# Optimization experiments

Hardware: AMD Instinct MI355X
Metric: run time of the kernel (lower is better)

The kernel has to match this reference:

```python
import jax, jax.numpy as jnp
import numpy as np

B, P, H, NO, NA = 8, 16, 32, 32, 8
D, L, NH, F = 768, 12, 12, 3072
DH = D // NH
N = P + H * (NO + NA)  # 1296
NEG = -1e9


def _rule_mask():
    # group ids: 0=task(prefix), 1=obs, 2=action; prefix timestep = -1
    g = np.concatenate([np.zeros(P, np.int32),
                        np.tile(np.concatenate([np.full(NO, 1, np.int32), np.full(NA, 2, np.int32)]), H)])
    t = np.concatenate([np.full(P, -1, np.int32), np.repeat(np.arange(H, dtype=np.int32), NO + NA)])
    ti, tj = t[:, None], t[None, :]
    # attention_rules: everyone attends ALL to task; obs/action attend CAUSAL to obs;
    # action attends CAUSAL to action; task attends ALL to task; all else NEVER.
    rules = {(0, 0): 'all', (1, 0): 'all', (2, 0): 'all',
             (1, 1): 'causal', (2, 1): 'causal', (2, 2): 'causal'}
    m = np.zeros((N, N), bool)
    for (gi, gj), r in rules.items():
        sel = (g[:, None] == gi) & (g[None, :] == gj)
        cond = np.ones((N, N), bool) if r == 'all' else (tj <= ti)
        m |= sel & cond
    return m

RULE_MASK = jnp.asarray(_rule_mask())
SCALE = np.float32(1.0 / np.sqrt(DH))


def _ln(x, s, b):
    mu = x.mean(-1, keepdims=True)
    var = ((x - mu) ** 2).mean(-1, keepdims=True)
    return (x - mu) * jax.lax.rsqrt(var + 1e-6) * s + b


def _forward(prefix_tokens, obs_tokens, act_tokens, ln1_s, ln1_b, ln2_s, ln2_b,
             wq, wk, wv, wo, bq, bk, bv, bo, w1, b1, w2, b2, lnf_s, lnf_b,
             prefix_mask, obs_mask, act_mask):
    # assemble_input_tokens: concat timestep groups on token dim, fold horizon, prepend prefix
    ts = jnp.concatenate([obs_tokens, act_tokens], axis=2).reshape(B, H * (NO + NA), D)
    x = jnp.concatenate([prefix_tokens, ts], axis=1)  # (B, N, D)
    pad = jnp.concatenate(
        [prefix_mask, jnp.concatenate([obs_mask, act_mask], axis=2).reshape(B, -1)], axis=1)
    mask = RULE_MASK[None, None] & pad[:, None, None, :]  # (B,1,N,N), broadcast over heads
    for i in range(L):
        h = _ln(x, ln1_s[i], ln1_b[i])
        q = (h @ wq[i] + bq[i]).reshape(B, N, NH, DH)
        k = (h @ wk[i] + bk[i]).reshape(B, N, NH, DH)
        v = (h @ wv[i] + bv[i]).reshape(B, N, NH, DH)
        s = jnp.einsum('bqhd,bkhd->bhqk', q, k) * SCALE
        a = jax.nn.softmax(jnp.where(mask, s, NEG), axis=-1)
        o = jnp.einsum('bhqk,bkhd->bqhd', a, v).reshape(B, N, D)
        x = x + o @ wo[i] + bo[i]
        h2 = _ln(x, ln2_s[i], ln2_b[i])
        x = x + jax.nn.gelu(h2 @ w1[i] + b1[i]) @ w2[i] + b2[i]
    return _ln(x, lnf_s, lnf_b)


def setup_inputs() -> dict:
    key = jax.random.key(0)
    ks = jax.random.split(key, 9)
    sc = 0.02
    return dict(
        prefix_tokens=jax.random.normal(ks[0], (B, P, D), jnp.float32),
        obs_tokens=jax.random.normal(ks[1], (B, H, NO, D), jnp.float32),
        act_tokens=jax.random.normal(ks[2], (B, H, NA, D), jnp.float32),
        ln1_s=jnp.ones((L, D), jnp.float32), ln1_b=jnp.zeros((L, D), jnp.float32),
        ln2_s=jnp.ones((L, D), jnp.float32), ln2_b=jnp.zeros((L, D), jnp.float32),
        wq=jax.random.normal(ks[3], (L, D, D), jnp.float32) * sc,
        wk=jax.random.normal(ks[4], (L, D, D), jnp.float32) * sc,
        wv=jax.random.normal(ks[5], (L, D, D), jnp.float32) * sc,
        wo=jax.random.normal(ks[6], (L, D, D), jnp.float32) * sc,
        bq=jnp.zeros((L, D), jnp.float32), bk=jnp.zeros((L, D), jnp.float32),
        bv=jnp.zeros((L, D), jnp.float32), bo=jnp.zeros((L, D), jnp.float32),
        w1=jax.random.normal(ks[7], (L, D, F), jnp.float32) * sc,
        b1=jnp.zeros((L, F), jnp.float32),
        w2=jax.random.normal(ks[8], (L, F, D), jnp.float32) * sc,
        b2=jnp.zeros((L, D), jnp.float32),
        lnf_s=jnp.ones((D,), jnp.float32), lnf_b=jnp.zeros((D,), jnp.float32),
        prefix_mask=jnp.ones((B, P), bool),
        obs_mask=jnp.ones((B, H, NO), bool),
        act_mask=jnp.ones((B, H, NA), bool),
    )


def reference(prefix_tokens, obs_tokens, act_tokens, ln1_s, ln1_b, ln2_s, ln2_b,
              wq, wk, wv, wo, bq, bk, bv, bo, w1, b1, w2, b2, lnf_s, lnf_b,
              prefix_mask, obs_mask, act_mask):
    return _forward(prefix_tokens, obs_tokens, act_tokens, ln1_s, ln1_b, ln2_s, ln2_b,
                    wq, wk, wv, wo, bq, bk, bv, bo, w1, b1, w2, b2, lnf_s, lnf_b,
                    prefix_mask, obs_mask, act_mask)
```

## Files before the change

kernel.cpp:

```cpp
#include <hip/hip_runtime.h>

typedef unsigned short u16;
typedef __attribute__((ext_vector_type(8))) __bf16 bf16x8;
typedef __attribute__((ext_vector_type(4))) float floatx4;

#define NTOK 1296
#define BN_TOT 10368
#define DMODEL 768
#define DFF 3072
#define NHEAD 12
#define DHEAD 64
#define NLAYER 12
#define NQT 21
#define SCALE_QK 0.125f

__device__ __forceinline__ u16 f2bf(float f) {
    unsigned u = __builtin_bit_cast(unsigned, f);
    unsigned r = (u + 0x7FFFu + ((u >> 16) & 1u)) >> 16;
    return (u16)r;
}

__device__ __forceinline__ float gelu_f(float x) {
    float u = 0.7978845608028654f * (x + 0.044715f * x * x * x);
    float t = 1.f - 2.f / (__expf(2.f * u) + 1.f);
    return 0.5f * x * (1.f + t);
}

template <int CTRL>
__device__ __forceinline__ float dpp_f(float x) {
    int r = __builtin_amdgcn_update_dpp(0, __builtin_bit_cast(int, x), CTRL, 0xF, 0xF, true);
    return __builtin_bit_cast(float, r);
}
__device__ __forceinline__ float red16_max(float x) {
    x = fmaxf(x, dpp_f<0xB1>(x));
    x = fmaxf(x, dpp_f<0x4E>(x));
    x = fmaxf(x, dpp_f<0x141>(x));
    x = fmaxf(x, dpp_f<0x140>(x));
    return x;
}
__device__ __forceinline__ float red16_sum(float x) {
    x += dpp_f<0xB1>(x);
    x += dpp_f<0x4E>(x);
    x += dpp_f<0x141>(x);
    x += dpp_f<0x140>(x);
    return x;
}

__global__ void assemble_x(const float* __restrict__ prefix,
                           const float* __restrict__ obs,
                           const float* __restrict__ act,
                           float* __restrict__ X) {
    int idx = blockIdx.x * 256 + threadIdx.x;
    if (idx >= BN_TOT * DMODEL) return;
    int d = idx % DMODEL;
    int n = (idx / DMODEL) % NTOK;
    int b = idx / (DMODEL * NTOK);
    float v;
    if (n < 16) {
        v = prefix[((size_t)b * 16 + n) * DMODEL + d];
    } else {
        int q = n - 16;
        int m = q / 40, r = q % 40;
        if (r < 32) v = obs[(((size_t)b * 32 + m) * 32 + r) * DMODEL + d];
        else        v = act[(((size_t)b * 32 + m) * 8 + (r - 32)) * DMODEL + d];
    }
    X[idx] = v;
}

__global__ void build_pad(const int* __restrict__ pm,
                          const int* __restrict__ om,
                          const int* __restrict__ am,
                          unsigned char* __restrict__ pad) {
    int idx = blockIdx.x * 256 + threadIdx.x;
    if (idx >= BN_TOT) return;
    int n = idx % NTOK, b = idx / NTOK;
    int v;
    if (n < 16) v = pm[b * 16 + n];
    else {
        int q = n - 16;
        int m = q / 40, r = q % 40;
        v = (r < 32) ? om[(b * 32 + m) * 32 + r] : am[(b * 32 + m) * 8 + (r - 32)];
    }
    pad[idx] = (v != 0) ? 1 : 0;
}

__global__ void transpose_cvt(const float* __restrict__ src, u16* __restrict__ dst,
                              int K, int Nc, long layerStride) {
    src += (size_t)blockIdx.z * K * Nc;
    dst += (size_t)blockIdx.z * layerStride;
    __shared__ float tile[32][33];
    int n0 = blockIdx.x * 32, k0 = blockIdx.y * 32;
    int tx = threadIdx.x, ty = threadIdx.y;
#pragma unroll
    for (int i = 0; i < 4; ++i)
        tile[ty + i * 8][tx] = src[(size_t)(k0 + ty + i * 8) * Nc + n0 + tx];
    __syncthreads();
#pragma unroll
    for (int i = 0; i < 4; ++i) {
        int n = n0 + ty + i * 8;
        dst[(size_t)n * K + k0 + tx] = f2bf(tile[tx][ty + i * 8]);
    }
}

__global__ __launch_bounds__(256) void ln_kernel(const float* __restrict__ x,
                                                 const float* __restrict__ s,
                                                 const float* __restrict__ bb,
                                                 u16* __restrict__ obf,
                                                 float* __restrict__ of32) {
    int row = blockIdx.x;
    const float* xr = x + (size_t)row * DMODEL;
    int t = threadIdx.x;
    float v0 = xr[t], v1 = xr[t + 256], v2 = xr[t + 512];
    float sum = v0 + v1 + v2;
    float sq = v0 * v0 + v1 * v1 + v2 * v2;
#pragma unroll
    for (int d = 32; d > 0; d >>= 1) {
        sum += __shfl_down(sum, d);
        sq  += __shfl_down(sq, d);
    }
    __shared__ float ps[8], pq[8];
    int w = t >> 6, lane = t & 63;
    if (lane == 0) { ps[w] = sum; pq[w] = sq; }
    __syncthreads();
    if (t == 0) {
        float S = ps[0] + ps[1] + ps[2] + ps[3];
        float Q = pq[0] + pq[1] + pq[2] + pq[3];
        float mu = S * (1.f / DMODEL);
        float var = Q * (1.f / DMODEL) - mu * mu;
        ps[4] = mu; pq[4] = rsqrtf(var + 1e-6f);
    }
    __syncthreads();
    float mu = ps[4], rs = pq[4];
#pragma unroll
    for (int i = 0; i < 3; ++i) {
        int col = t + i * 256;
        float v = (i == 0 ? v0 : (i == 1 ? v1 : v2));
        float y = (v - mu) * rs * s[col] + bb[col];
        if (obf) obf[(size_t)row * DMODEL + col] = f2bf(y);
        else     of32[(size_t)row * DMODEL + col] = y;
    }
}

template <int EPI>
__global__ __launch_bounds__(256) void gemm_k(const u16* __restrict__ A,
                                              const u16* __restrict__ Bt,
                                              const float* __restrict__ bias,
                                              const float* __restrict__ resid,
                                              void* __restrict__ outp,
                                              int M, int Nc, int K) {
    __shared__ __attribute__((aligned(16))) u16 As[4096];
    __shared__ __attribute__((aligned(16))) u16 Bs[4096];
    int tid = threadIdx.x;
    int bc = blockIdx.x, br = blockIdx.y;
    int lane = tid & 63, w = tid >> 6;
    int wr = (w >> 1) * 64, wc = (w & 1) * 64;
    int lr = lane & 15, C = lane >> 4;
    floatx4 acc[4][4] = {};

    int r0 = tid >> 2;
    int cph = tid & 3;
    const u16* Abase = A + (size_t)(br * 128) * K;
    const u16* Bbase = Bt + (size_t)(bc * 128) * K;

    for (int k0 = 0; k0 < K; k0 += 32) {
        __syncthreads();
#pragma unroll
        for (int i = 0; i < 2; ++i) {
            int r = i * 64 + r0;
            int cl = cph ^ ((r >> 1) & 3);
            const u16* ga = Abase + (size_t)r * K + k0 + cl * 8;
            const u16* gb = Bbase + (size_t)r * K + k0 + cl * 8;
            __builtin_amdgcn_global_load_lds(
                (const __attribute__((address_space(1))) void*)ga,
                (__attribute__((address_space(3))) void*)&As[(i * 256 + w * 64) * 8], 16, 0, 0);
            __builtin_amdgcn_global_load_lds(
                (const __attribute__((address_space(1))) void*)gb,
                (__attribute__((address_space(3))) void*)&Bs[(i * 256 + w * 64) * 8], 16, 0, 0);
        }
        __syncthreads();
        bf16x8 af[4], bf[4];
#pragma unroll
        for (int i = 0; i < 4; ++i) {
            int R = wr + i * 16 + lr;
            af[i] = *(const bf16x8*)&As[(R * 4 + (C ^ ((R >> 1) & 3))) * 8];
        }
#pragma unroll
        for (int i = 0; i < 4; ++i) {
            int R = wc + i * 16 + lr;
            bf[i] = *(const bf16x8*)&Bs[(R * 4 + (C ^ ((R >> 1) & 3))) * 8];
        }
#pragma unroll
        for (int i = 0; i < 4; ++i)
#pragma unroll
            for (int j = 0; j < 4; ++j)
                acc[i][j] = __builtin_amdgcn_mfma_f32_16x16x32_bf16(af[i], bf[j], acc[i][j], 0, 0, 0);
    }

    int gr0 = br * 128 + wr, gc0 = bc * 128 + wc;
#pragma unroll
    for (int i = 0; i < 4; ++i) {
#pragma unroll
        for (int j = 0; j < 4; ++j) {
#pragma unroll
            for (int r = 0; r < 4; ++r) {
                int grow = gr0 + i * 16 + (lane >> 4) * 4 + r;
                int gcol = gc0 + j * 16 + lr;
                float v = acc[i][j][r] + bias[gcol];
                if constexpr (EPI == 0) {
                    int b = grow / NTOK, n = grow % NTOK;
                    int nh = gcol >> 6, dh = gcol & 63;
                    ((u16*)outp)[(((size_t)b * NHEAD + nh) * NTOK + n) * DHEAD + dh] = f2bf(v);
                } else if constexpr (EPI == 1) {
                    int b = grow / NTOK, n = grow % NTOK;
                    int nh = gcol >> 6, dh = gcol & 63;
                    ((u16*)outp)[(((size_t)b * NHEAD + nh) * DHEAD + dh) * NTOK + n] = f2bf(v);
                } else if constexpr (EPI == 2) {
                    ((u16*)outp)[(size_t)grow * Nc + gcol] = f2bf(gelu_f(v));
                } else {
                    size_t idx = (size_t)grow * Nc + gcol;
                    ((float*)outp)[idx] = resid[idx] + v;
                }
            }
        }
    }
}

__global__ __launch_bounds__(256) void attn_k(const u16* __restrict__ Q,
                                              const u16* __restrict__ Kb,
                                              const u16* __restrict__ Vt,
                                              const unsigned char* __restrict__ pad,
                                              u16* __restrict__ O) {
    __shared__ __attribute__((aligned(16))) u16 plds[4][16 * 72];
    int wgid = blockIdx.x;
    int xcd = wgid & 7, slot = wgid >> 3;
    int qt = slot % NQT;
    int g = (slot / NQT) * 8 + xcd;
    int b = g / NHEAD, h = g % NHEAD;

    int tid = threadIdx.x, lane = tid & 63, w = tid >> 6;
    int rg = lane >> 4, lc = lane & 15;
    int q0 = qt * 64 + w * 16;
    size_t bh = (size_t)(b * NHEAD + h);

    int lastrow = min(qt * 64 + 63, NTOK - 1);
    int jend = (lastrow < 16) ? 16 : 16 + 40 * ((lastrow - 16) / 40 + 1);
    jend = min(jend, NTOK);
    int njt = (jend + 63) >> 6;

    int tmax_obs[4], tmax_act[4];
    bool rowok[4];
#pragma unroll
    for (int r = 0; r < 4; ++r) {
        int row = q0 + rg * 4 + r;
        rowok[r] = (row < NTOK);
        if (row >= 16 && row < NTOK) {
            int qi = row - 16;
            int ti = qi / 40;
            bool gact = (qi % 40) >= 32;
            tmax_obs[r] = ti;
            tmax_act[r] = gact ? ti : -1;
        } else {
            tmax_obs[r] = -1;
            tmax_act[r] = -1;
        }
    }

    const u16* qb = Q + (bh * NTOK + min(q0 + lc, NTOK - 1)) * DHEAD;
    bf16x8 qf0, qf1;
    {
        bf16x8 t0 = *(const bf16x8*)(qb + rg * 8);
        bf16x8 t1 = *(const bf16x8*)(qb + 32 + rg * 8);
#pragma unroll
        for (int i = 0; i < 8; ++i) {
            qf0[i] = (__bf16)((float)t0[i] * SCALE_QK);
            qf1[i] = (__bf16)((float)t1[i] * SCALE_QK);
        }
    }

    floatx4 oacc[4] = {};
    float mi[4] = {-3.0e38f, -3.0e38f, -3.0e38f, -3.0e38f};
    float li[4] = {0.f, 0.f, 0.f, 0.f};
    const unsigned char* padb = pad + (size_t)b * NTOK;

    for (int jt = 0; jt < njt; ++jt) {
        int j0 = jt * 64;
        floatx4 s[4];
#pragma unroll
        for (int ct = 0; ct < 4; ++ct) {
            int keyc = min(j0 + ct * 16 + lc, NTOK - 1);
            const u16* kb = Kb + (bh * NTOK + keyc) * DHEAD;
            bf16x8 kf0 = *(const bf16x8*)(kb + rg * 8);
            bf16x8 kf1 = *(const bf16x8*)(kb + 32 + rg * 8);
            floatx4 sa = {};
            sa = __builtin_amdgcn_mfma_f32_16x16x32_bf16(qf0, kf0, sa, 0, 0, 0);
            sa = __builtin_amdgcn_mfma_f32_16x16x32_bf16(qf1, kf1, sa, 0, 0, 0);
            s[ct] = sa;
        }
#pragma unroll
        for (int ct = 0; ct < 4; ++ct) {
            int col = j0 + ct * 16 + lc;
            bool colok = (col < jend) && (padb[min(col, NTOK - 1)] != 0);
            bool jpre = (col < 16);
            int tj = 0; bool jact = false;
            if (!jpre) { int qj = col - 16; tj = qj / 40; jact = (qj % 40) >= 32; }
#pragma unroll
            for (int r = 0; r < 4; ++r) {
                int tm = jact ? tmax_act[r] : tmax_obs[r];
                bool ok = colok && rowok[r] && (jpre || tj <= tm);
                s[ct][r] = ok ? s[ct][r] : -1.0e9f;
            }
        }
#pragma unroll
        for (int r = 0; r < 4; ++r) {
            float mx = fmaxf(fmaxf(s[0][r], s[1][r]), fmaxf(s[2][r], s[3][r]));
            mx = red16_max(mx);
            float mnew = fmaxf(mi[r], mx);
            float alpha = __expf(mi[r] - mnew);
            float rs = 0.f;
#pragma unroll
            for (int ct = 0; ct < 4; ++ct) {
                float p = __expf(s[ct][r] - mnew);
                s[ct][r] = p;
                rs += p;
            }
            rs = red16_sum(rs);
            li[r] = li[r] * alpha + rs;
            mi[r] = mnew;
#pragma unroll
            for (int ct = 0; ct < 4; ++ct) oacc[ct][r] *= alpha;
        }
#pragma unroll
        for (int ct = 0; ct < 4; ++ct)
#pragma unroll
            for (int r = 0; r < 4; ++r)
                plds[w][(rg * 4 + r) * 72 + ct * 16 + lc] = f2bf(s[ct][r]);
        bf16x8 pf0 = *(const bf16x8*)&plds[w][lc * 72 + rg * 8];
        bf16x8 pf1 = *(const bf16x8*)&plds[w][lc * 72 + 32 + rg * 8];
#pragma unroll
        for (int ct = 0; ct < 4; ++ct) {
            const u16* vb = Vt + (bh * DHEAD + ct * 16 + lc) * NTOK + j0;
            bf16x8 vf0 = *(const bf16x8*)(vb + rg * 8);
            bf16x8 vf1 = *(const bf16x8*)(vb + 32 + rg * 8);
            oacc[ct] = __builtin_amdgcn_mfma_f32_16x16x32_bf16(pf0, vf0, oacc[ct], 0, 0, 0);
            oacc[ct] = __builtin_amdgcn_mfma_f32_16x16x32_bf16(pf1, vf1, oacc[ct], 0, 0, 0);
        }
    }
#pragma unroll
    for (int r = 0; r < 4; ++r) {
        int row = q0 + rg * 4 + r;
        if (row < NTOK) {
            float inv = 1.f / li[r];
#pragma unroll
            for (int ct = 0; ct < 4; ++ct)
                O[((size_t)b * NTOK + row) * DMODEL + h * DHEAD + ct * 16 + lc] = f2bf(oacc[ct][r] * inv);
        }
    }
}

extern "C" void kernel_launch(void* const* d_in, const int* in_sizes, int n_in,
                              void* d_out, int out_size, void* d_ws, size_t ws_size,
                              hipStream_t stream) {
    const float* prefix = (const float*)d_in[0];
    const float* obs    = (const float*)d_in[1];
    const float* act    = (const float*)d_in[2];
    const float* ln1_s  = (const float*)d_in[3];
    const float* ln1_b  = (const float*)d_in[4];
    const float* ln2_s  = (const float*)d_in[5];
    const float* ln2_b  = (const float*)d_in[6];
    const float* wq = (const float*)d_in[7];
    const float* wk = (const float*)d_in[8];
    const float* wv = (const float*)d_in[9];
    const float* wo = (const float*)d_in[10];
    const float* bq = (const float*)d_in[11];
    const float* bk = (const float*)d_in[12];
    const float* bv = (const float*)d_in[13];
    const float* bo = (const float*)d_in[14];
    const float* w1 = (const float*)d_in[15];
    const float* b1 = (const float*)d_in[16];
    const float* w2 = (const float*)d_in[17];
    const float* b2 = (const float*)d_in[18];
    const float* lnf_s = (const float*)d_in[19];
    const float* lnf_b = (const float*)d_in[20];
    const int* pm = (const int*)d_in[21];
    const int* om = (const int*)d_in[22];
    const int* am = (const int*)d_in[23];
    float* out = (float*)d_out;

    char* ws = (char*)d_ws;
    size_t off = 0;
    auto carve = [&](size_t bytes) -> char* {
        char* p = ws + off;
        off += (bytes + 255) & ~(size_t)255;
        return p;
    };
    float* X   = (float*)carve((size_t)BN_TOT * DMODEL * 4);
    u16*   Hb  = (u16*)carve((size_t)BN_TOT * DMODEL * 2);
    u16*   Qb  = (u16*)carve((size_t)BN_TOT * DMODEL * 2);
    u16*   Kbf = (u16*)carve((size_t)BN_TOT * DMODEL * 2);
    u16*   Vt  = (u16*)carve((size_t)BN_TOT * DMODEL * 2 + 256);
    u16*   Ob  = (u16*)carve((size_t)BN_TOT * DMODEL * 2);
    u16*   MID = (u16*)carve((size_t)BN_TOT * DFF * 2);
    unsigned char* PAD = (unsigned char*)carve(BN_TOT);
    u16*   WT  = (u16*)carve((size_t)NLAYER * 7077888 * 2);
    if (off > ws_size) return;

    const long LSTR = 7077888;
    const long OWQ = 0, OWK = 589824, OWV = 1179648, OWO = 1769472, OW1 = 2359296, OW2 = 4718592;

    dim3 blk(256);
    assemble_x<<<(BN_TOT * DMODEL + 255) / 256, blk, 0, stream>>>(prefix, obs, act, X);
    build_pad<<<(BN_TOT + 255) / 256, blk, 0, stream>>>(pm, om, am, PAD);

    dim3 tb(32, 8);
    transpose_cvt<<<dim3(DMODEL / 32, DMODEL / 32, NLAYER), tb, 0, stream>>>(wq, WT + OWQ, DMODEL, DMODEL, LSTR);
    transpose_cvt<<<dim3(DMODEL / 32, DMODEL / 32, NLAYER), tb, 0, stream>>>(wk, WT + OWK, DMODEL, DMODEL, LSTR);
    transpose_cvt<<<dim3(DMODEL / 32, DMODEL / 32, NLAYER), tb, 0, stream>>>(wv, WT + OWV, DMODEL, DMODEL, LSTR);
    transpose_cvt<<<dim3(DMODEL / 32, DMODEL / 32, NLAYER), tb, 0, stream>>>(wo, WT + OWO, DMODEL, DMODEL, LSTR);
    transpose_cvt<<<dim3(DFF / 32, DMODEL / 32, NLAYER), tb, 0, stream>>>(w1, WT + OW1, DMODEL, DFF, LSTR);
    transpose_cvt<<<dim3(DMODEL / 32, DFF / 32, NLAYER), tb, 0, stream>>>(w2, WT + OW2, DFF, DMODEL, LSTR);

    dim3 g6(DMODEL / 128, BN_TOT / 128);
    dim3 g24(DFF / 128, BN_TOT / 128);
    dim3 ga(NQT * NHEAD * 8);

    for (int l = 0; l < NLAYER; ++l) {
        const u16* WTl = WT + (size_t)l * LSTR;
        ln_kernel<<<BN_TOT, blk, 0, stream>>>(X, ln1_s + l * DMODEL, ln1_b + l * DMODEL, Hb, nullptr);
        gemm_k<0><<<g6, blk, 0, stream>>>(Hb, WTl + OWQ, bq + l * DMODEL, nullptr, Qb, BN_TOT, DMODEL, DMODEL);
        gemm_k<0><<<g6, blk, 0, stream>>>(Hb, WTl + OWK, bk + l * DMODEL, nullptr, Kbf, BN_TOT, DMODEL, DMODEL);
        gemm_k<1><<<g6, blk, 0, stream>>>(Hb, WTl + OWV, bv + l * DMODEL, nullptr, Vt, BN_TOT, DMODEL, DMODEL);
        attn_k<<<ga, blk, 0, stream>>>(Qb, Kbf, Vt, PAD, Ob);
        gemm_k<3><<<g6, blk, 0, stream>>>(Ob, WTl + OWO, bo + l * DMODEL, X, X, BN_TOT, DMODEL, DMODEL);
        ln_kernel<<<BN_TOT, blk, 0, stream>>>(X, ln2_s + l * DMODEL, ln2_b + l * DMODEL, Hb, nullptr);
        gemm_k<2><<<g24, blk, 0, stream>>>(Hb, WTl + OW1, b1 + l * DFF, nullptr, MID, BN_TOT, DFF, DMODEL);
        gemm_k<3><<<g6, blk, 0, stream>>>(MID, WTl + OW2, b2 + l * DMODEL, X, X, BN_TOT, DMODEL, DFF);
    }
    ln_kernel<<<BN_TOT, blk, 0, stream>>>(X, lnf_s, lnf_b, nullptr, out);
}
```

Measured before the change: 6.488 ms.

## Fuse QKV projections, transpose attention MFMA layout, vectorize layernorm rows per wave

Merges the three Q/K/V GEMMs into one wider GEMM, using the contiguous WQ/WK/WV weight layout and a concatenated bias, so the normed activations are read once and there are fewer launches. Attention swaps the MFMA operand order so each lane owns one query row. That replaces the DPP row reductions with two cross-lane shuffles, adds packed bf16 conversion, and uses a swizzled P tile in LDS plus reversed query-tile order to schedule the heavier causal tiles first. Layernorm now handles one row per wave with float4 loads and no block barriers. Several independent changes land at once, which raises the risk of a correctness slip in the masking or layout logic.

Result: faster. 6.313 ms (-2.7%).

```diff
diff --git a/kernel.cpp b/kernel.cpp
--- a/kernel.cpp
+++ b/kernel.cpp
@@ -20,30 +20,16 @@
     return (u16)r;
 }
 
+__device__ __forceinline__ unsigned cvt_pk_bf16(float lo, float hi) {
+    unsigned r;
+    asm("v_cvt_pk_bf16_f32 %0, %1, %2" : "=v"(r) : "v"(lo), "v"(hi));
+    return r;
+}
+
 __device__ __forceinline__ float gelu_f(float x) {
     float u = 0.7978845608028654f * (x + 0.044715f * x * x * x);
     float t = 1.f - 2.f / (__expf(2.f * u) + 1.f);
     return 0.5f * x * (1.f + t);
-}
-
-template <int CTRL>
-__device__ __forceinline__ float dpp_f(float x) {
-    int r = __builtin_amdgcn_update_dpp(0, __builtin_bit_cast(int, x), CTRL, 0xF, 0xF, true);
-    return __builtin_bit_cast(float, r);
-}
-__device__ __forceinline__ float red16_max(float x) {
-    x = fmaxf(x, dpp_f<0xB1>(x));
-    x = fmaxf(x, dpp_f<0x4E>(x));
-    x = fmaxf(x, dpp_f<0x141>(x));
-    x = fmaxf(x, dpp_f<0x140>(x));
-    return x;
-}
-__device__ __forceinline__ float red16_sum(float x) {
-    x += dpp_f<0xB1>(x);
-    x += dpp_f<0x4E>(x);
-    x += dpp_f<0x141>(x);
-    x += dpp_f<0x140>(x);
-    return x;
 }
 
 __global__ void assemble_x(const float* __restrict__ prefix,
@@ -84,6 +70,18 @@
     pad[idx] = (v != 0) ? 1 : 0;
 }
 
+__global__ void build_biascat(const float* __restrict__ bq,
+                              const float* __restrict__ bk,
+                              const float* __restrict__ bv,
+                              float* __restrict__ bc) {
+    int idx = blockIdx.x * 256 + threadIdx.x;
+    if (idx >= NLAYER * 2304) return;
+    int l = idx / 2304, c = idx % 2304;
+    int which = c / 768, cc = c % 768;
+    const float* src = (which == 0) ? bq : (which == 1) ? bk : bv;
+    bc[idx] = src[l * 768 + cc];
+}
+
 __global__ void transpose_cvt(const float* __restrict__ src, u16* __restrict__ dst,
                               int K, int Nc, long layerStride) {
     src += (size_t)blockIdx.z * K * Nc;
@@ -107,37 +105,44 @@
                                                  const float* __restrict__ bb,
                                                  u16* __restrict__ obf,
                                                  float* __restrict__ of32) {
-    int row = blockIdx.x;
-    const float* xr = x + (size_t)row * DMODEL;
-    int t = threadIdx.x;
-    float v0 = xr[t], v1 = xr[t + 256], v2 = xr[t + 512];
-    float sum = v0 + v1 + v2;
-    float sq = v0 * v0 + v1 * v1 + v2 * v2;
+    int row = blockIdx.x * 4 + (threadIdx.x >> 6);
+    int lane = threadIdx.x & 63;
+    const float4* xv = (const float4*)(x + (size_t)row * DMODEL);
+    float4 v[3];
+    v[0] = xv[lane]; v[1] = xv[lane + 64]; v[2] = xv[lane + 128];
+    float sum = 0.f, sq = 0.f;
+#pragma unroll
+    for (int i = 0; i < 3; ++i) {
+        sum += v[i].x + v[i].y + v[i].z + v[i].w;
+        sq  += v[i].x * v[i].x + v[i].y * v[i].y + v[i].z * v[i].z + v[i].w * v[i].w;
+    }
 #pragma unroll
     for (int d = 32; d > 0; d >>= 1) {
-        sum += __shfl_down(sum, d);
-        sq  += __shfl_down(sq, d);
-    }
-    __shared__ float ps[8], pq[8];
-    int w = t >> 6, lane = t & 63;
-    if (lane == 0) { ps[w] = sum; pq[w] = sq; }
-    __syncthreads();
-    if (t == 0) {
-        float S = ps[0] + ps[1] + ps[2] + ps[3];
-        float Q = pq[0] + pq[1] + pq[2] + pq[3];
-        float mu = S * (1.f / DMODEL);
-        float var = Q * (1.f / DMODEL) - mu * mu;
-        ps[4] = mu; pq[4] = rsqrtf(var + 1e-6f);
-    }
-    __syncthreads();
-    float mu = ps[4], rs = pq[4];
+        sum += __shfl_xor(sum, d);
+        sq  += __shfl_xor(sq, d);
+    }
+    float mu = sum * (1.f / DMODEL);
+    float var = sq * (1.f / DMODEL) - mu * mu;
+    float rstd = rsqrtf(var + 1e-6f);
+    const float4* sv = (const float4*)s;
+    const float4* bv = (const float4*)bb;
 #pragma unroll
     for (int i = 0; i < 3; ++i) {
-        int col = t + i * 256;
-        float v = (i == 0 ? v0 : (i == 1 ? v1 : v2));
-        float y = (v - mu) * rs * s[col] + bb[col];
-        if (obf) obf[(size_t)row * DMODEL + col] = f2bf(y);
-        else     of32[(size_t)row * DMODEL + col] = y;
+        float4 sc = sv[lane + i * 64], bc = bv[lane + i * 64];
+        float y0 = (v[i].x - mu) * rstd * sc.x + bc.x;
+        float y1 = (v[i].y - mu) * rstd * sc.y + bc.y;
+        float y2 = (v[i].z - mu) * rstd * sc.z + bc.z;
+        float y3 = (v[i].w - mu) * rstd * sc.w + bc.w;
+        size_t base = (size_t)row * DMODEL + i * 256 + lane * 4;
+        if (obf) {
+            uint2 pk;
+            pk.x = (unsigned)f2bf(y0) | ((unsigned)f2bf(y1) << 16);
+            pk.y = (unsigned)f2bf(y2) | ((unsigned)f2bf(y3) << 16);
+            *(uint2*)&obf[base] = pk;
+        } else {
+            float4 o = {y0, y1, y2, y3};
+            *(float4*)&of32[base] = o;
+        }
     }
 }
 
@@ -206,19 +211,21 @@
                 int grow = gr0 + i * 16 + (lane >> 4) * 4 + r;
                 int gcol = gc0 + j * 16 + lr;
                 float v = acc[i][j][r] + bias[gcol];
-                if constexpr (EPI == 0) {
-                    int b = grow / NTOK, n = grow % NTOK;
-                    int nh = gcol >> 6, dh = gcol & 63;
-                    ((u16*)outp)[(((size_t)b * NHEAD + nh) * NTOK + n) * DHEAD + dh] = f2bf(v);
-                } else if constexpr (EPI == 1) {
-                    int b = grow / NTOK, n = grow % NTOK;
-                    int nh = gcol >> 6, dh = gcol & 63;
-                    ((u16*)outp)[(((size_t)b * NHEAD + nh) * DHEAD + dh) * NTOK + n] = f2bf(v);
-                } else if constexpr (EPI == 2) {
+                if constexpr (EPI == 2) {
                     ((u16*)outp)[(size_t)grow * Nc + gcol] = f2bf(gelu_f(v));
-                } else {
+                } else if constexpr (EPI == 3) {
                     size_t idx = (size_t)grow * Nc + gcol;
                     ((float*)outp)[idx] = resid[idx] + v;
+                } else {
+                    int b = grow / NTOK, n = grow % NTOK;
+                    int which = gcol / 768;
+                    int c = gcol - which * 768;
+                    int nh = c >> 6, dh = c & 63;
+                    u16* base = (u16*)outp + (size_t)which * ((size_t)BN_TOT * DMODEL);
+                    if (which < 2)
+                        base[(((size_t)b * NHEAD + nh) * NTOK + n) * DHEAD + dh] = f2bf(v);
+                    else
+                        base[(((size_t)b * NHEAD + nh) * DHEAD + dh) * NTOK + n] = f2bf(v);
                 }
             }
         }
@@ -230,10 +237,10 @@
                                               const u16* __restrict__ Vt,
                                               const unsigned char* __restrict__ pad,
                                               u16* __restrict__ O) {
-    __shared__ __attribute__((aligned(16))) u16 plds[4][16 * 72];
+    __shared__ __attribute__((aligned(16))) u16 plds[4][16 * 64];
     int wgid = blockIdx.x;
     int xcd = wgid & 7, slot = wgid >> 3;
-    int qt = slot % NQT;
+    int qt = NQT - 1 - (slot % NQT);
     int g = (slot / NQT) * 8 + xcd;
     int b = g / NHEAD, h = g % NHEAD;
 
@@ -247,25 +254,18 @@
     jend = min(jend, NTOK);
     int njt = (jend + 63) >> 6;
 
-    int tmax_obs[4], tmax_act[4];
-    bool rowok[4];
-#pragma unroll
-    for (int r = 0; r < 4; ++r) {
-        int row = q0 + rg * 4 + r;
-        rowok[r] = (row < NTOK);
-        if (row >= 16 && row < NTOK) {
-            int qi = row - 16;
-            int ti = qi / 40;
-            bool gact = (qi % 40) >= 32;
-            tmax_obs[r] = ti;
-            tmax_act[r] = gact ? ti : -1;
-        } else {
-            tmax_obs[r] = -1;
-            tmax_act[r] = -1;
-        }
-    }
-
-    const u16* qb = Q + (bh * NTOK + min(q0 + lc, NTOK - 1)) * DHEAD;
+    int q = q0 + lc;
+    bool qok = q < NTOK;
+    int tmax_obs = -1, tmax_act = -1;
+    if (qok && q >= 16) {
+        int qi = q - 16;
+        int ti = qi / 40;
+        bool gact = (qi % 40) >= 32;
+        tmax_obs = ti;
+        tmax_act = gact ? ti : -1;
+    }
+
+    const u16* qb = Q + (bh * NTOK + min(q, NTOK - 1)) * DHEAD;
     bf16x8 qf0, qf1;
     {
         bf16x8 t0 = *(const bf16x8*)(qb + rg * 8);
@@ -278,8 +278,7 @@
     }
 
     floatx4 oacc[4] = {};
-    float mi[4] = {-3.0e38f, -3.0e38f, -3.0e38f, -3.0e38f};
-    float li[4] = {0.f, 0.f, 0.f, 0.f};
+    float mi = -3.0e38f, li = 0.f;
     const unsigned char* padb = pad + (size_t)b * NTOK;
 
     for (int jt = 0; jt < njt; ++jt) {
@@ -292,67 +291,87 @@
             bf16x8 kf0 = *(const bf16x8*)(kb + rg * 8);
             bf16x8 kf1 = *(const bf16x8*)(kb + 32 + rg * 8);
             floatx4 sa = {};
-            sa = __builtin_amdgcn_mfma_f32_16x16x32_bf16(qf0, kf0, sa, 0, 0, 0);
-            sa = __builtin_amdgcn_mfma_f32_16x16x32_bf16(qf1, kf1, sa, 0, 0, 0);
+            sa = __builtin_amdgcn_mfma_f32_16x16x32_bf16(kf0, qf0, sa, 0, 0, 0);
+            sa = __builtin_amdgcn_mfma_f32_16x16x32_bf16(kf1, qf1, sa, 0, 0, 0);
             s[ct] = sa;
         }
 #pragma unroll
         for (int ct = 0; ct < 4; ++ct) {
-            int col = j0 + ct * 16 + lc;
-            bool colok = (col < jend) && (padb[min(col, NTOK - 1)] != 0);
-            bool jpre = (col < 16);
-            int tj = 0; bool jact = false;
-            if (!jpre) { int qj = col - 16; tj = qj / 40; jact = (qj % 40) >= 32; }
+            int kb0 = j0 + ct * 16 + rg * 4;
+            unsigned pw = (kb0 < NTOK) ? *(const unsigned*)(padb + kb0) : 0u;
+            bool jpre = kb0 < 16;
+            int tj0 = 0, rem0 = 0;
+            if (!jpre) { int qj = kb0 - 16; tj0 = qj / 40; rem0 = qj - 40 * tj0; }
 #pragma unroll
             for (int r = 0; r < 4; ++r) {
-                int tm = jact ? tmax_act[r] : tmax_obs[r];
-                bool ok = colok && rowok[r] && (jpre || tj <= tm);
+                int key = kb0 + r;
+                bool colok = qok && (key < jend) && (((pw >> (8 * r)) & 0xFFu) != 0);
+                bool ok;
+                if (jpre) ok = colok;
+                else {
+                    int rem = rem0 + r;
+                    int tj = tj0 + (rem >= 40 ? 1 : 0);
+                    int remr = rem >= 40 ? rem - 40 : rem;
+                    int tm = (remr >= 32) ? tmax_act : tmax_obs;
+                    ok = colok && (tj <= tm);
+                }
                 s[ct][r] = ok ? s[ct][r] : -1.0e9f;
             }
         }
-#pragma unroll
-        for (int r = 0; r < 4; ++r) {
-            float mx = fmaxf(fmaxf(s[0][r], s[1][r]), fmaxf(s[2][r], s[3][r]));
-            mx = red16_max(mx);
-            float mnew = fmaxf(mi[r], mx);
-            float alpha = __expf(mi[r] - mnew);
-            float rs = 0.f;
-#pragma unroll
-            for (int ct = 0; ct < 4; ++ct) {
+        float mt = fmaxf(fmaxf(fmaxf(s[0][0], s[0][1]), fmaxf(s[0][2], s[0][3])),
+                         fmaxf(fmaxf(s[1][0], s[1][1]), fmaxf(s[1][2], s[1][3])));
+        float mt2 = fmaxf(fmaxf(fmaxf(s[2][0], s[2][1]), fmaxf(s[2][2], s[2][3])),
+                          fmaxf(fmaxf(s[3][0], s[3][1]), fmaxf(s[3][2], s[3][3])));
+        mt = fmaxf(mt, mt2);
+        mt = fmaxf(mt, __shfl_xor(mt, 16));
+        mt = fmaxf(mt, __shfl_xor(mt, 32));
+        float mnew = fmaxf(mi, mt);
+        float alpha = __expf(mi - mnew);
+        float rs = 0.f;
+#pragma unroll
+        for (int ct = 0; ct < 4; ++ct)
+#pragma unroll
+            for (int r = 0; r < 4; ++r) {
                 float p = __expf(s[ct][r] - mnew);
                 s[ct][r] = p;
                 rs += p;
             }
-            rs = red16_sum(rs);
-            li[r] = li[r] * alpha + rs;
-            mi[r] = mnew;
-#pragma unroll
-            for (int ct = 0; ct < 4; ++ct) oacc[ct][r] *= alpha;
-        }
+        rs += __shfl_xor(rs, 16);
+        rs += __shfl_xor(rs, 32);
+        li = li * alpha + rs;
+        mi = mnew;
 #pragma unroll
         for (int ct = 0; ct < 4; ++ct)
 #pragma unroll
-            for (int r = 0; r < 4; ++r)
-                plds[w][(rg * 4 + r) * 72 + ct * 16 + lc] = f2bf(s[ct][r]);
-        bf16x8 pf0 = *(const bf16x8*)&plds[w][lc * 72 + rg * 8];
-        bf16x8 pf1 = *(const bf16x8*)&plds[w][lc * 72 + 32 + rg * 8];
+            for (int r = 0; r < 4; ++r) oacc[ct][r] *= alpha;
 #pragma unroll
         for (int ct = 0; ct < 4; ++ct) {
-            const u16* vb = Vt + (bh * DHEAD + ct * 16 + lc) * NTOK + j0;
-            bf16x8 vf0 = *(const bf16x8*)(vb + rg * 8);
-            bf16x8 vf1 = *(const bf16x8*)(vb + 32 + rg * 8);
-            oacc[ct] = __builtin_amdgcn_mfma_f32_16x16x32_bf16(pf0, vf0, oacc[ct], 0, 0, 0);
-            oacc[ct] = __builtin_amdgcn_mfma_f32_16x16x32_bf16(pf1, vf1, oacc[ct], 0, 0, 0);
-        }
-    }
-#pragma unroll
-    for (int r = 0; r < 4; ++r) {
-        int row = q0 + rg * 4 + r;
-        if (row < NTOK) {
-            float inv = 1.f / li[r];
-#pragma unroll
-            for (int ct = 0; ct < 4; ++ct)
-                O[((size_t)b * NTOK + row) * DMODEL + h * DHEAD + ct * 16 + lc] = f2bf(oacc[ct][r] * inv);
+            uint2 pk;
+            pk.x = cvt_pk_bf16(s[ct][0], s[ct][1]);
+            pk.y = cvt_pk_bf16(s[ct][2], s[ct][3]);
+            int chunk = 2 * ct + (rg >> 1);
+            int idx = lc * 64 + ((chunk ^ (lc & 7)) << 3) + ((rg & 1) << 2);
+            *(uint2*)&plds[w][idx] = pk;
+        }
+#pragma unroll
+        for (int kh = 0; kh < 2; ++kh) {
+            bf16x8 pf = *(const bf16x8*)&plds[w][lc * 64 + (((4 * kh + rg) ^ (lc & 7)) << 3)];
+#pragma unroll
+            for (int ct = 0; ct < 4; ++ct) {
+                const u16* vb = Vt + (bh * DHEAD + ct * 16 + lc) * NTOK + j0 + kh * 32;
+                bf16x8 vf = *(const bf16x8*)(vb + rg * 8);
+                oacc[ct] = __builtin_amdgcn_mfma_f32_16x16x32_bf16(vf, pf, oacc[ct], 0, 0, 0);
+            }
+        }
+    }
+    if (q < NTOK) {
+        float inv = 1.f / li;
+#pragma unroll
+        for (int ct = 0; ct < 4; ++ct) {
+            uint2 pk;
+            pk.x = cvt_pk_bf16(oacc[ct][0] * inv, oacc[ct][1] * inv);
+            pk.y = cvt_pk_bf16(oacc[ct][2] * inv, oacc[ct][3] * inv);
+            *(uint2*)&O[((size_t)b * NTOK + q) * DMODEL + h * DHEAD + ct * 16 + rg * 4] = pk;
         }
     }
 }
@@ -395,21 +414,25 @@
     };
     float* X   = (float*)carve((size_t)BN_TOT * DMODEL * 4);
     u16*   Hb  = (u16*)carve((size_t)BN_TOT * DMODEL * 2);
-    u16*   Qb  = (u16*)carve((size_t)BN_TOT * DMODEL * 2);
-    u16*   Kbf = (u16*)carve((size_t)BN_TOT * DMODEL * 2);
-    u16*   Vt  = (u16*)carve((size_t)BN_TOT * DMODEL * 2 + 256);
+    u16*   QKV = (u16*)carve((size_t)3 * BN_TOT * DMODEL * 2);
+    u16*   Qb  = QKV;
+    u16*   Kbf = QKV + (size_t)BN_TOT * DMODEL;
+    u16*   Vt  = QKV + (size_t)2 * BN_TOT * DMODEL;
     u16*   Ob  = (u16*)carve((size_t)BN_TOT * DMODEL * 2);
     u16*   MID = (u16*)carve((size_t)BN_TOT * DFF * 2);
     unsigned char* PAD = (unsigned char*)carve(BN_TOT);
+    float* BIASC = (float*)carve((size_t)NLAYER * 2304 * 4);
     u16*   WT  = (u16*)carve((size_t)NLAYER * 7077888 * 2);
     if (off > ws_size) return;
 
     const long LSTR = 7077888;
-    const long OWQ = 0, OWK = 589824, OWV = 1179648, OWO = 1769472, OW1 = 2359296, OW2 = 4718592;
+    const long OWQ = 0, OWO = 1769472, OW1 = 2359296, OW2 = 4718592;
+    const long OWK = 589824, OWV = 1179648;
 
     dim3 blk(256);
     assemble_x<<<(BN_TOT * DMODEL + 255) / 256, blk, 0, stream>>>(prefix, obs, act, X);
     build_pad<<<(BN_TOT + 255) / 256, blk, 0, stream>>>(pm, om, am, PAD);
+    build_biascat<<<(NLAYER * 2304 + 255) / 256, blk, 0, stream>>>(bq, bk, bv, BIASC);
 
     dim3 tb(32, 8);
     transpose_cvt<<<dim3(DMODEL / 32, DMODEL / 32, NLAYER), tb, 0, stream>>>(wq, WT + OWQ, DMODEL, DMODEL, LSTR);
@@ -420,20 +443,20 @@
     transpose_cvt<<<dim3(DMODEL / 32, DFF / 32, NLAYER), tb, 0, stream>>>(w2, WT + OW2, DFF, DMODEL, LSTR);
 
     dim3 g6(DMODEL / 128, BN_TOT / 128);
+    dim3 gqkv(2304 / 128, BN_TOT / 128);
     dim3 g24(DFF / 128, BN_TOT / 128);
     dim3 ga(NQT * NHEAD * 8);
+    dim3 gln(BN_TOT / 4);
 
     for (int l = 0; l < NLAYER; ++l) {
         const u16* WTl = WT + (size_t)l * LSTR;
-        ln_kernel<<<BN_TOT, blk, 0, stream>>>(X, ln1_s + l * DMODEL, ln1_b + l * DMODEL, Hb, nullptr);
-        gemm_k<0><<<g6, blk, 0, stream>>>(Hb, WTl + OWQ, bq + l * DMODEL, nullptr, Qb, BN_TOT, DMODEL, DMODEL);
-        gemm_k<0><<<g6, blk, 0, stream>>>(Hb, WTl + OWK, bk + l * DMODEL, nullptr, Kbf, BN_TOT, DMODEL, DMODEL);
-        gemm_k<1><<<g6, blk, 0, stream>>>(Hb, WTl + OWV, bv + l * DMODEL, nullptr, Vt, BN_TOT, DMODEL, DMODEL);
+        ln_kernel<<<gln, blk, 0, stream>>>(X, ln1_s + l * DMODEL, ln1_b + l * DMODEL, Hb, nullptr);
+        gemm_k<4><<<gqkv, blk, 0, stream>>>(Hb, WTl + OWQ, BIASC + l * 2304, nullptr, Qb, BN_TOT, 2304, DMODEL);
         attn_k<<<ga, blk, 0, stream>>>(Qb, Kbf, Vt, PAD, Ob);
         gemm_k<3><<<g6, blk, 0, stream>>>(Ob, WTl + OWO, bo + l * DMODEL, X, X, BN_TOT, DMODEL, DMODEL);
-        ln_kernel<<<BN_TOT, blk, 0, stream>>>(X, ln2_s + l * DMODEL, ln2_b + l * DMODEL, Hb, nullptr);
+        ln_kernel<<<gln, blk, 0, stream>>>(X, ln2_s + l * DMODEL, ln2_b + l * DMODEL, Hb, nullptr);
         gemm_k<2><<<g24, blk, 0, stream>>>(Hb, WTl + OW1, b1 + l * DFF, nullptr, MID, BN_TOT, DFF, DMODEL);
         gemm_k<3><<<g6, blk, 0, stream>>>(MID, WTl + OW2, b2 + l * DMODEL, X, X, BN_TOT, DMODEL, DFF);
     }
-    ln_kernel<<<BN_TOT, blk, 0, stream>>>(X, lnf_s, lnf_b, nullptr, out);
-}
+    ln_kernel<<<gln, blk, 0, stream>>>(X, lnf_s, lnf_b, nullptr, out);
+}
```
